# Kernel tuning notes

Hardware: AMD Instinct MI355X
Metric: run time of the kernel (lower is better)

The kernel has to match this reference:

```python
import jax, jax.numpy as jnp
import numpy as np

EPS = 1e-5  # BatchNorm2d default eps


def setup_inputs() -> dict:
    key = jax.random.key(0)
    k1, k2, k3, k4 = jax.random.split(key, 4)
    B, C, S, E = 2, 512, 256, 512  # C == E is required by the module's math
    x = jax.random.normal(k1, (B, C, S, E), dtype=jnp.float32)
    Q = jax.random.normal(k2, (E, E), dtype=jnp.float32)
    K = jax.random.normal(k3, (E, E), dtype=jnp.float32)
    V = jax.random.normal(k4, (E, E), dtype=jnp.float32)
    return {"x": x, "Q": Q, "K": K, "V": V}


def reference(x, Q, K, V):
    # BatchNorm2d(affine=False), training-mode batch stats over (B, H, W)
    mean = jnp.mean(x, axis=(0, 2, 3), keepdims=True)
    var = jnp.var(x, axis=(0, 2, 3), keepdims=True)  # biased, matches torch normalization
    xn = (x - mean) * jax.lax.rsqrt(var + EPS)

    divisor = jnp.sqrt(jnp.asarray(x.shape[-1], dtype=x.dtype))
    q = jnp.einsum('bcse,ef->bcsf', xn, Q)
    k = jnp.einsum('bcse,ef->bcsf', xn, K)
    v = jnp.einsum('bcse,ef->bcsf', xn, V)

    # scores: [B, C, S, S]
    prod = jnp.einsum('bcsf,bctf->bcst', q, k) / divisor
    # nn.Softmax2d softmaxes over the CHANNEL dim (axis 1)
    sm = jax.nn.softmax(prod, axis=1)
    attention = jnp.einsum('bcst,bctf->bcsf', sm, v)
    # dropout is identity in eval/reference mode; residual since E_in == E_out
    return attention + xn
```

## Files before the change

kernel.cpp:

```cpp
#include <hip/hip_runtime.h>
#include <hip/hip_bf16.h>
#include <cstdio>

#define Bn 2
#define Cn 512
#define Sn 256
#define En 512

typedef __attribute__((ext_vector_type(8))) short bf16x8;
typedef __attribute__((ext_vector_type(4))) float f32x4;

static constexpr size_t PROD_B = (1ull << 20);
static constexpr size_t V_B    = PROD_B + (256ull << 20);
static constexpr size_t ATH_B  = V_B + (256ull << 20);
static constexpr size_t ATL_B  = ATH_B + (512ull << 10);
static constexpr size_t VT_B   = ATL_B + (512ull << 10);
static constexpr size_t XNH_B  = VT_B + (512ull << 10);
static constexpr size_t XNL_B  = XNH_B + (256ull << 20);
static constexpr size_t WS_BIG = XNL_B + (256ull << 20);
static constexpr size_t SMT_B  = XNL_B;

__device__ __forceinline__ unsigned short f2bf(float f) {
  union { __hip_bfloat16 h; unsigned short u; } cv;
  cv.h = __float2bfloat16(f);
  return cv.u;
}
__device__ __forceinline__ float bf2f(unsigned short u) {
  union { unsigned int i; float f; } cv;
  cv.i = ((unsigned int)u) << 16;
  return cv.f;
}
__device__ __forceinline__ void split2(float v, unsigned short& h, unsigned short& l) {
  h = f2bf(v);
  l = f2bf(v - bf2f(h));
}
__device__ __forceinline__ bf16x8 ldfrag(const unsigned short* arr, int row, int ks, int lane) {
  const int byte = (ks * 64 + ((lane >> 4) << 4)) ^ ((row & 7) << 4);
  return *(const bf16x8*)((const char*)(arr + (size_t)row * 64) + byte);
}
__device__ __forceinline__ f32x4 MFMA(bf16x8 a, bf16x8 b, f32x4 c) {
  return __builtin_amdgcn_mfma_f32_16x16x32_bf16(a, b, c, 0, 0, 0);
}
__device__ __forceinline__ void glds16(const void* g, void* l) {
  __builtin_amdgcn_global_load_lds(
      (const __attribute__((address_space(1))) unsigned int*)g,
      (__attribute__((address_space(3))) unsigned int*)l, 16, 0, 0);
}
__device__ __forceinline__ void stage_tile(const unsigned short* g, unsigned short* l,
                                           int nbytes, int wid, int lane, int nwaves) {
  const char* gb = (const char*)g;
  char* lb = (char*)l;
  for (int j = wid; j < (nbytes >> 10); j += nwaves)
    glds16(gb + j * 1024 + lane * 16, lb + j * 1024);
}

__global__ void k1_stats(const float* __restrict__ x, float* __restrict__ ws) {
  const int c = blockIdx.x, tid = threadIdx.x;
  const float4* p0 = (const float4*)(x + (size_t)c * (Sn * En));
  const float4* p1 = (const float4*)(x + (size_t)(Cn + c) * (Sn * En));
  float s1 = 0.f, s2 = 0.f;
  for (int i = tid; i < (Sn * En / 4); i += 256) {
    float4 a = p0[i], b = p1[i];
    s1 += (a.x + a.y) + (a.z + a.w) + (b.x + b.y) + (b.z + b.w);
    s2 += (a.x * a.x + a.y * a.y) + (a.z * a.z + a.w * a.w) +
          (b.x * b.x + b.y * b.y) + (b.z * b.z + b.w * b.w);
  }
  __shared__ float r1[256], r2[256];
  r1[tid] = s1; r2[tid] = s2;
  __syncthreads();
  for (int off = 128; off > 0; off >>= 1) {
    if (tid < off) { r1[tid] += r1[tid + off]; r2[tid] += r2[tid + off]; }
    __syncthreads();
  }
  if (tid == 0) {
    const float n = (float)(2 * Sn * En);
    float mean = r1[0] / n;
    float var = r2[0] / n - mean * mean;
    ws[c] = mean;
    ws[512 + c] = 1.0f / sqrtf(var + 1e-5f);
  }
}

__global__ void kA(const float* __restrict__ Q, const float* __restrict__ K,
                   const float* __restrict__ V, unsigned short* __restrict__ ATh,
                   unsigned short* __restrict__ ATl, unsigned short* __restrict__ VT) {
  const int f = blockIdx.x, tid = threadIdx.x;
  __shared__ float Kf[512];
  for (int i = tid; i < 512; i += 256) Kf[i] = K[(size_t)f * 512 + i];
  __syncthreads();
  const int fr64 = f & 63;
  const size_t atbase = ((size_t)(f >> 6) * 8) * 4096 + (size_t)fr64 * 64;
  const size_t vtbase = ((size_t)(f >> 7) * 8) * 8192 + (size_t)(f & 127) * 64;
#pragma unroll
  for (int half = 0; half < 2; ++half) {
    const int e = tid + half * 256;
    const float* Qe = Q + (size_t)e * 512;
    float acc = 0.f;
    for (int t = 0; t < 512; t += 4) {
      float4 q = *(const float4*)(Qe + t);
      acc += q.x * Kf[t] + q.y * Kf[t + 1] + q.z * Kf[t + 2] + q.w * Kf[t + 3];
    }
    unsigned short h, l;
    split2(acc, h, l);
    const int et = e >> 6, ec = e & 63;
    const int swa = (ec & 3) | ((ec & 60) ^ ((fr64 & 7) << 3));
    ATh[atbase + (size_t)et * 4096 + swa] = h;
    ATl[atbase + (size_t)et * 4096 + swa] = l;
    const int swv = (ec & 3) | ((ec & 60) ^ ((f & 7) << 3));
    VT[vtbase + (size_t)et * 8192 + swv] = f2bf(V[(size_t)e * 512 + f]);
  }
}

__global__ void kxn(const float* __restrict__ x, const float* __restrict__ ws,
                    unsigned short* __restrict__ XNh, unsigned short* __restrict__ XNl) {
  const int bid = blockIdx.x;
  const int bc = bid >> 1, half = bid & 1;
  const int c = bc & 511;
  const float mean = ws[c], rstd = ws[512 + c];
  const float* xb = x + (size_t)bc * 131072 + (size_t)half * 128 * 512;
  const int tid = threadIdx.x;
#pragma unroll 4
  for (int i = 0; i < 64; ++i) {
    const int g = tid + i * 256;
    const int r = g >> 7, c4 = g & 127;
    const float4 xv = *(const float4*)(xb + (size_t)r * 512 + c4 * 4);
    ushort4 hv, lv;
    split2((xv.x - mean) * rstd, hv.x, lv.x);
    split2((xv.y - mean) * rstd, hv.y, lv.y);
    split2((xv.z - mean) * rstd, hv.z, lv.z);
    split2((xv.w - mean) * rstd, hv.w, lv.w);
    const int et = c4 >> 4, colt4 = c4 & 15;
    const int row = half * 128 + r;
    const size_t idx = ((size_t)(bc * 8 + et) * 256 + row) * 64 +
                       ((colt4 * 4) ^ ((row & 7) << 3));
    *(ushort4*)&XNh[idx] = hv;
    *(ushort4*)&XNl[idx] = lv;
  }
}

__launch_bounds__(256)
__global__ void kv_proj(const unsigned short* __restrict__ VT,
                        const unsigned short* __restrict__ XNh_g,
                        unsigned short* __restrict__ vT_out) {
  __shared__ unsigned short BUF[2][16384];
  const int bid = blockIdx.x;
  const int L = (bid & 7) * 1024 + (bid >> 3);
  const int bc = L >> 3;
  const int fq = (L >> 1) & 3;
  const int th = L & 1;
  const int f0 = fq * 128, t0 = th * 128;
  const int tid = threadIdx.x, w = tid >> 6, lane = tid & 63;

  f32x4 acc[2][8];
#pragma unroll
  for (int i = 0; i < 2; ++i)
#pragma unroll
    for (int j = 0; j < 8; ++j) acc[i][j] = (f32x4){0.f, 0.f, 0.f, 0.f};

  stage_tile(VT + ((size_t)fq * 8 + 0) * 8192, &BUF[0][0], 16384, w, lane, 4);
  stage_tile(XNh_g + ((size_t)(bc * 8 + 0) * 256 + t0) * 64, &BUF[0][8192], 16384, w, lane, 4);
  __syncthreads();
#pragma unroll 1
  for (int et = 0; et < 8; ++et) {
    if (et < 7) {
      const int b = (et + 1) & 1;
      stage_tile(VT + ((size_t)fq * 8 + et + 1) * 8192, &BUF[b][0], 16384, w, lane, 4);
      stage_tile(XNh_g + ((size_t)(bc * 8 + et + 1) * 256 + t0) * 64, &BUF[b][8192],
                 16384, w, lane, 4);
    }
    const unsigned short* cb = &BUF[et & 1][0];
#pragma unroll
    for (int ks = 0; ks < 2; ++ks) {
      bf16x8 a0 = ldfrag(cb, w * 32 + (lane & 15), ks, lane);
      bf16x8 a1 = ldfrag(cb, w * 32 + 16 + (lane & 15), ks, lane);
#pragma unroll
      for (int ct = 0; ct < 8; ++ct) {
        bf16x8 b = ldfrag(cb + 8192, ct * 16 + (lane & 15), ks, lane);
        acc[0][ct] = MFMA(a0, b, acc[0][ct]);
        acc[1][ct] = MFMA(a1, b, acc[1][ct]);
      }
    }
    __syncthreads();
  }
#pragma unroll
  for (int rt = 0; rt < 2; ++rt)
#pragma unroll
    for (int ct = 0; ct < 8; ++ct)
#pragma unroll
      for (int r = 0; r < 4; ++r) {
        const int f = f0 + w * 32 + rt * 16 + (lane >> 4) * 4 + r;
        const int t = t0 + ct * 16 + (lane & 15);
        const size_t idx = (((size_t)bc * 4 + (f >> 7)) * 4 + (t >> 6)) * 8192 +
                           (size_t)(f & 127) * 64 +
                           ((t & 3) | ((t & 60) ^ ((f & 7) << 3)));
        vT_out[idx] = f2bf(acc[rt][ct][r]);
      }
}

__launch_bounds__(512)
__global__ void kscores(const unsigned short* __restrict__ ATh_g,
                        const unsigned short* __restrict__ ATl_g,
                        const unsigned short* __restrict__ XNh_g,
                        const unsigned short* __restrict__ XNl_g,
                        float* __restrict__ prod) {
  __shared__ unsigned short ATS[32768];
  __shared__ unsigned short XNS[32768];
  __shared__ unsigned short YS[8][1024];
  const int bid = blockIdx.x;
  const int L = (bid & 7) * 256 + (bid >> 3);
  const int bc = L >> 1, half = L & 1;
  float* prodc = prod + (size_t)bc * 65536 + (size_t)half * 128 * 256;
  const int tid = threadIdx.x, w = tid >> 6, lane = tid & 63;
  const int lr = lane & 15, lk = lane >> 4;

  const int arow = half * 128 + w * 16 + lr;
  const unsigned short* xnh_row = XNh_g + ((size_t)bc * 8 * 256 + arow) * 64;
  const unsigned short* xnl_row = XNl_g + ((size_t)bc * 8 * 256 + arow) * 64;
  const int ac0 = ((lk * 8)) ^ ((arow & 7) << 3);
  const int ac1 = (32 + lk * 8) ^ ((arow & 7) << 3);

  f32x4 accz[16];
#pragma unroll
  for (int i = 0; i < 16; ++i) accz[i] = (f32x4){0.f, 0.f, 0.f, 0.f};
  f32x4 accy[2];
  unsigned short* const ys = &YS[w][0];

  auto stATS = [&](int j) {
    const int ft64 = j >> 1, hf = (j & 1) * 2048;
    const char* gh = (const char*)(ATh_g + ((size_t)ft64 * 8 + w) * 4096 + hf);
    const char* gl = (const char*)(ATl_g + ((size_t)ft64 * 8 + w) * 4096 + hf);
    char* dh = (char*)(ATS + w * 2048);
    char* dl = (char*)(ATS + 16384 + w * 2048);
#pragma unroll
    for (int r = 0; r < 4; ++r) {
      glds16(gh + r * 1024 + lane * 16, dh + r * 1024);
      glds16(gl + r * 1024 + lane * 16, dl + r * 1024);
    }
  };
  auto stXNS = [&](int fe) {
    const char* gh = (const char*)(XNh_g + (size_t)(bc * 8 + fe) * 16384);
    const char* gl = (const char*)(XNl_g + (size_t)(bc * 8 + fe) * 16384);
#pragma unroll
    for (int r = 0; r < 4; ++r) {
      glds16(gh + (w * 4 + r) * 1024 + lane * 16, (char*)XNS + (w * 4 + r) * 1024);
      glds16(gl + (w * 4 + r) * 1024 + lane * 16, (char*)(XNS + 16384) + (w * 4 + r) * 1024);
    }
  };
  auto ph1 = [&]() {
#pragma unroll 2
    for (int et = 0; et < 8; ++et) {
      const unsigned short* ATSh = ATS + et * 2048;
      const unsigned short* ATSl = ATS + 16384 + et * 2048;
#pragma unroll
      for (int ks = 0; ks < 2; ++ks) {
        const int ac = (ks ? ac1 : ac0);
        const bf16x8 ah = *(const bf16x8*)(xnh_row + (size_t)et * 16384 + ac);
        const bf16x8 al = *(const bf16x8*)(xnl_row + (size_t)et * 16384 + ac);
#pragma unroll
        for (int fc = 0; fc < 2; ++fc) {
          bf16x8 bh = ldfrag(ATSh, fc * 16 + lr, ks, lane);
          bf16x8 bl = ldfrag(ATSl, fc * 16 + lr, ks, lane);
          accy[fc] = MFMA(ah, bh, accy[fc]);
          accy[fc] = MFMA(ah, bl, accy[fc]);
          accy[fc] = MFMA(al, bh, accy[fc]);
        }
      }
    }
  };
  auto ywrite = [&]() {
#pragma unroll
    for (int fc = 0; fc < 2; ++fc)
#pragma unroll
      for (int r = 0; r < 4; ++r) {
        unsigned short h, l;
        split2(accy[fc][r], h, l);
        const int idx = (lk * 4 + r) * 32 + fc * 16 + lr;
        ys[idx] = h;
        ys[512 + idx] = l;
      }
  };
  auto ph2 = [&](int j) {
    const int jo = (j & 1) * 64;
    const bf16x8 yh = *(const bf16x8*)((const char*)ys + lr * 64 + lk * 16);
    const bf16x8 yl = *(const bf16x8*)((const char*)ys + 1024 + lr * 64 + lk * 16);
#pragma unroll
    for (int ct = 0; ct < 16; ++ct) {
      const int t = ct * 16 + lr;
      const int byte = (jo + lk * 16) ^ ((t & 7) << 4);
      const bf16x8 bh = *(const bf16x8*)((const char*)(XNS + (size_t)t * 64) + byte);
      const bf16x8 bl = *(const bf16x8*)((const char*)(XNS + 16384 + (size_t)t * 64) + byte);
      accz[ct] = MFMA(yh, bh, accz[ct]);
      accz[ct] = MFMA(yh, bl, accz[ct]);
      accz[ct] = MFMA(yl, bh, accz[ct]);
    }
  };

  stXNS(0);
  stATS(0);
  __syncthreads();

#pragma unroll 1
  for (int fe = 0; fe < 8; ++fe) {
    accy[0] = (f32x4){0.f, 0.f, 0.f, 0.f};
    accy[1] = (f32x4){0.f, 0.f, 0.f, 0.f};
    ph1();
    ywrite();
    __syncthreads();
    stATS(2 * fe + 1);
    ph2(2 * fe);
    __syncthreads();
    accy[0] = (f32x4){0.f, 0.f, 0.f, 0.f};
    accy[1] = (f32x4){0.f, 0.f, 0.f, 0.f};
    ph1();
    ywrite();
    __syncthreads();
    if (fe < 7) stATS(2 * fe + 2);
    ph2(2 * fe + 1);
    __syncthreads();
    if (fe < 7) stXNS(fe + 1);
  }

  const float scale = 0.044194173824159216f;
#pragma unroll
  for (int ct = 0; ct < 16; ++ct)
#pragma unroll
    for (int r = 0; r < 4; ++r) {
      const int row = w * 16 + lk * 4 + r;
      prodc[(size_t)row * 256 + ct * 16 + lr] = accz[ct][r] * scale;
    }
}

__launch_bounds__(512)
__global__ void k3_softmax(const float* __restrict__ prodf, unsigned short* __restrict__ smT) {
  const int bid = blockIdx.x;
  const int b = bid >> 8, s = bid & 255;
  const int tid = threadIdx.x;
  const int t = tid & 255, ch = tid >> 8;
  const float* __restrict__ p =
      prodf + (size_t)b * (512ull * 65536) + (size_t)s * 256 + t + (size_t)ch * 256 * 65536;
  float m = -3.4e38f, sum = 0.f;
#pragma unroll 4
  for (int cc = 0; cc < 256; ++cc) {
    const float v = p[(size_t)cc * 65536];
    if (v > m) { sum *= __expf(m - v); m = v; }
    sum += __expf(v - m);
  }
  __shared__ float Ms[2][256], Ss[2][256];
  Ms[ch][t] = m; Ss[ch][t] = sum;
  __syncthreads();
  const float mo = Ms[ch ^ 1][t], so = Ss[ch ^ 1][t];
  const float mm = fmaxf(m, mo);
  const float inv = 1.0f / (sum * __expf(m - mm) + so * __expf(mo - mm));
  const int sh = s >> 7, r = s & 127, kt = t >> 6, col = t & 63;
  const int cidx = r * 64 + ((col & 3) | ((col & 60) ^ ((r & 7) << 3)));
  const size_t tbase = ((size_t)b * 512 + ch * 256) * 2 + sh;
#pragma unroll 4
  for (int cc = 0; cc < 256; ++cc) {
    const float ev = __expf(p[(size_t)cc * 65536] - mm) * inv;
    smT[((tbase + (size_t)cc * 2) * 4 + kt) * 8192 + cidx] = f2bf(ev);
  }
}

__launch_bounds__(256)
__global__ void k4_pv(const unsigned short* __restrict__ XNh_g,
                      const unsigned short* __restrict__ vT,
                      const unsigned short* __restrict__ smT,
                      float* __restrict__ out) {
  __shared__ unsigned short BUF[2][16384];
  const int bid = blockIdx.x;
  const int L = (bid & 7) * 1024 + (bid >> 3);
  const int bc = L >> 3;
  const int sh = (L >> 2) & 1;
  const int fh = L & 3;
  const int s0 = sh * 128, f0 = fh * 128;
  const int tid = threadIdx.x, w = tid >> 6, lane = tid & 63;

  f32x4 acc[2][8];
#pragma unroll
  for (int i = 0; i < 2; ++i)
#pragma unroll
    for (int j = 0; j < 8; ++j) acc[i][j] = (f32x4){0.f, 0.f, 0.f, 0.f};

  stage_tile(smT + (((size_t)bc * 2 + sh) * 4 + 0) * 8192, &BUF[0][0], 16384, w, lane, 4);
  stage_tile(vT + (((size_t)bc * 4 + fh) * 4 + 0) * 8192, &BUF[0][8192], 16384, w, lane, 4);
  __syncthreads();
#pragma unroll 1
  for (int kt = 0; kt < 4; ++kt) {
    if (kt < 3) {
      const int b = (kt + 1) & 1;
      stage_tile(smT + (((size_t)bc * 2 + sh) * 4 + kt + 1) * 8192, &BUF[b][0],
                 16384, w, lane, 4);
      stage_tile(vT + (((size_t)bc * 4 + fh) * 4 + kt + 1) * 8192, &BUF[b][8192],
                 16384, w, lane, 4);
    }
    const unsigned short* cb = &BUF[kt & 1][0];
#pragma unroll
    for (int ks = 0; ks < 2; ++ks) {
      bf16x8 a0 = ldfrag(cb, w * 32 + (lane & 15), ks, lane);
      bf16x8 a1 = ldfrag(cb, w * 32 + 16 + (lane & 15), ks, lane);
#pragma unroll
      for (int ct = 0; ct < 8; ++ct) {
        bf16x8 b = ldfrag(cb + 8192, ct * 16 + (lane & 15), ks, lane);
        acc[0][ct] = MFMA(a0, b, acc[0][ct]);
        acc[1][ct] = MFMA(a1, b, acc[1][ct]);
      }
    }
    __syncthreads();
  }
  const int lr = lane & 15, lk = lane >> 4;
#pragma unroll
  for (int rt = 0; rt < 2; ++rt)
#pragma unroll
    for (int ct = 0; ct < 8; ++ct)
#pragma unroll
      for (int r = 0; r < 4; ++r) {
        const int srow = s0 + w * 32 + rt * 16 + lk * 4 + r;
        const int fcol = f0 + ct * 16 + lr;
        const int et = fcol >> 6, col = fcol & 63;
        const unsigned short xh = XNh_g[((size_t)(bc * 8 + et) * 256 + srow) * 64 +
                                        ((col & 3) | ((col & 60) ^ ((srow & 7) << 3)))];
        const size_t oi = (size_t)bc * 131072 + (size_t)srow * 512 + fcol;
        out[oi] = acc[rt][ct][r] + bf2f(xh);
      }
}

extern "C" void kernel_launch(void* const* d_in, const int* in_sizes, int n_in,
                              void* d_out, int out_size, void* d_ws, size_t ws_size,
                              hipStream_t stream) {
  const float* x = (const float*)d_in[0];
  const float* Q = (const float*)d_in[1];
  const float* K = (const float*)d_in[2];
  const float* V = (const float*)d_in[3];
  float* out = (float*)d_out;
  float* ws = (float*)d_ws;
  float* prodf = (float*)((char*)d_ws + PROD_B);
  unsigned short* vT   = (unsigned short*)((char*)d_ws + V_B);
  unsigned short* ATh  = (unsigned short*)((char*)d_ws + ATH_B);
  unsigned short* ATl  = (unsigned short*)((char*)d_ws + ATL_B);
  unsigned short* VTm  = (unsigned short*)((char*)d_ws + VT_B);
  unsigned short* XNh  = (unsigned short*)((char*)d_ws + XNH_B);
  unsigned short* XNl  = (unsigned short*)((char*)d_ws + XNL_B);
  unsigned short* smT  = (unsigned short*)((char*)d_ws + SMT_B);
  if (ws_size < WS_BIG) {
    fprintf(stderr, "kernel_launch: ws_size %zu < needed %zu — expect corruption\n",
            ws_size, WS_BIG);
  }
  k1_stats<<<dim3(512), dim3(256), 0, stream>>>(x, ws);
  kA<<<dim3(512), dim3(256), 0, stream>>>(Q, K, V, ATh, ATl, VTm);
  kxn<<<dim3(2048), dim3(256), 0, stream>>>(x, ws, XNh, XNl);
  kv_proj<<<dim3(8192), dim3(256), 0, stream>>>(VTm, XNh, vT);
  kscores<<<dim3(2048), dim3(512), 0, stream>>>(ATh, ATl, XNh, XNl, prodf);
  k3_softmax<<<dim3(512), dim3(512), 0, stream>>>(prodf, smT);
  k4_pv<<<dim3(8192), dim3(256), 0, stream>>>(XNh, vT, smT, out);
}
```

Measured before the change: 2.317 ms.

## Restructure kscores: double-buffer XN tiles, read AT from global, widen per-wave f-chunk

The scores kernel no longer stages the A^T weight tiles in shared memory. Each wave reads its B fragments directly from global/L2 and computes a 64-wide f chunk per pass instead of 32. The XN tile is now double-buffered in LDS, so the next tile is prefetched during compute, and the per-wave Y scratch uses a swizzled layout with priority raised around the MFMA loop. This removes about three of the four barriers per iteration and overlaps staging with math, at the cost of more global-load traffic and latency for the weight fragments plus doubled XN LDS usage.

```diff
diff --git a/kernel.cpp b/kernel.cpp
--- a/kernel.cpp
+++ b/kernel.cpp
@@ -203,8 +203,7 @@
                         const unsigned short* __restrict__ XNh_g,
                         const unsigned short* __restrict__ XNl_g,
                         float* __restrict__ prod) {
-  __shared__ unsigned short ATS[32768];
-  __shared__ unsigned short XNS[32768];
+  __shared__ unsigned short XNS[2][32768];
   __shared__ unsigned short YS[8][1024];
   const int bid = blockIdx.x;
   const int L = (bid & 7) * 256 + (bid >> 3);
@@ -216,108 +215,82 @@
   const int arow = half * 128 + w * 16 + lr;
   const unsigned short* xnh_row = XNh_g + ((size_t)bc * 8 * 256 + arow) * 64;
   const unsigned short* xnl_row = XNl_g + ((size_t)bc * 8 * 256 + arow) * 64;
-  const int ac0 = ((lk * 8)) ^ ((arow & 7) << 3);
+  const int ac0 = (lk * 8) ^ ((arow & 7) << 3);
   const int ac1 = (32 + lk * 8) ^ ((arow & 7) << 3);
+  const int brswz = (lr & 7) << 3;
 
   f32x4 accz[16];
 #pragma unroll
   for (int i = 0; i < 16; ++i) accz[i] = (f32x4){0.f, 0.f, 0.f, 0.f};
-  f32x4 accy[2];
+  f32x4 accy[4];
   unsigned short* const ys = &YS[w][0];
 
-  auto stATS = [&](int j) {
-    const int ft64 = j >> 1, hf = (j & 1) * 2048;
-    const char* gh = (const char*)(ATh_g + ((size_t)ft64 * 8 + w) * 4096 + hf);
-    const char* gl = (const char*)(ATl_g + ((size_t)ft64 * 8 + w) * 4096 + hf);
-    char* dh = (char*)(ATS + w * 2048);
-    char* dl = (char*)(ATS + 16384 + w * 2048);
-#pragma unroll
-    for (int r = 0; r < 4; ++r) {
-      glds16(gh + r * 1024 + lane * 16, dh + r * 1024);
-      glds16(gl + r * 1024 + lane * 16, dl + r * 1024);
-    }
+  auto stXNS = [&](int ft, int p) {
+    stage_tile(XNh_g + (size_t)(bc * 8 + ft) * 16384, &XNS[p][0], 32768, w, lane, 8);
+    stage_tile(XNl_g + (size_t)(bc * 8 + ft) * 16384, &XNS[p][16384], 32768, w, lane, 8);
   };
-  auto stXNS = [&](int fe) {
-    const char* gh = (const char*)(XNh_g + (size_t)(bc * 8 + fe) * 16384);
-    const char* gl = (const char*)(XNl_g + (size_t)(bc * 8 + fe) * 16384);
-#pragma unroll
-    for (int r = 0; r < 4; ++r) {
-      glds16(gh + (w * 4 + r) * 1024 + lane * 16, (char*)XNS + (w * 4 + r) * 1024);
-      glds16(gl + (w * 4 + r) * 1024 + lane * 16, (char*)(XNS + 16384) + (w * 4 + r) * 1024);
-    }
-  };
-  auto ph1 = [&]() {
+
+  stXNS(0, 0);
+  __syncthreads();
+
+#pragma unroll 1
+  for (int ft = 0; ft < 8; ++ft) {
+    if (ft < 7) stXNS(ft + 1, (ft + 1) & 1);
+#pragma unroll
+    for (int i = 0; i < 4; ++i) accy[i] = (f32x4){0.f, 0.f, 0.f, 0.f};
+
 #pragma unroll 2
     for (int et = 0; et < 8; ++et) {
-      const unsigned short* ATSh = ATS + et * 2048;
-      const unsigned short* ATSl = ATS + 16384 + et * 2048;
+      const unsigned short* ATh_t = ATh_g + ((size_t)ft * 8 + et) * 4096;
+      const unsigned short* ATl_t = ATl_g + ((size_t)ft * 8 + et) * 4096;
 #pragma unroll
       for (int ks = 0; ks < 2; ++ks) {
-        const int ac = (ks ? ac1 : ac0);
+        const int ac = ks ? ac1 : ac0;
         const bf16x8 ah = *(const bf16x8*)(xnh_row + (size_t)et * 16384 + ac);
         const bf16x8 al = *(const bf16x8*)(xnl_row + (size_t)et * 16384 + ac);
-#pragma unroll
-        for (int fc = 0; fc < 2; ++fc) {
-          bf16x8 bh = ldfrag(ATSh, fc * 16 + lr, ks, lane);
-          bf16x8 bl = ldfrag(ATSl, fc * 16 + lr, ks, lane);
+        const int bko = (ks * 32 + lk * 8) ^ brswz;
+#pragma unroll
+        for (int fc = 0; fc < 4; ++fc) {
+          const int bidx = (fc * 16 + lr) * 64 + bko;
+          const bf16x8 bh = *(const bf16x8*)(ATh_t + bidx);
+          const bf16x8 bl = *(const bf16x8*)(ATl_t + bidx);
           accy[fc] = MFMA(ah, bh, accy[fc]);
           accy[fc] = MFMA(ah, bl, accy[fc]);
           accy[fc] = MFMA(al, bh, accy[fc]);
         }
       }
     }
-  };
-  auto ywrite = [&]() {
-#pragma unroll
-    for (int fc = 0; fc < 2; ++fc)
-#pragma unroll
-      for (int r = 0; r < 4; ++r) {
-        unsigned short h, l;
-        split2(accy[fc][r], h, l);
-        const int idx = (lk * 4 + r) * 32 + fc * 16 + lr;
-        ys[idx] = h;
-        ys[512 + idx] = l;
-      }
-  };
-  auto ph2 = [&](int j) {
-    const int jo = (j & 1) * 64;
-    const bf16x8 yh = *(const bf16x8*)((const char*)ys + lr * 64 + lk * 16);
-    const bf16x8 yl = *(const bf16x8*)((const char*)ys + 1024 + lr * 64 + lk * 16);
-#pragma unroll
-    for (int ct = 0; ct < 16; ++ct) {
-      const int t = ct * 16 + lr;
-      const int byte = (jo + lk * 16) ^ ((t & 7) << 4);
-      const bf16x8 bh = *(const bf16x8*)((const char*)(XNS + (size_t)t * 64) + byte);
-      const bf16x8 bl = *(const bf16x8*)((const char*)(XNS + 16384 + (size_t)t * 64) + byte);
-      accz[ct] = MFMA(yh, bh, accz[ct]);
-      accz[ct] = MFMA(yh, bl, accz[ct]);
-      accz[ct] = MFMA(yl, bh, accz[ct]);
-    }
-  };
-
-  stXNS(0);
-  stATS(0);
-  __syncthreads();
-
-#pragma unroll 1
-  for (int fe = 0; fe < 8; ++fe) {
-    accy[0] = (f32x4){0.f, 0.f, 0.f, 0.f};
-    accy[1] = (f32x4){0.f, 0.f, 0.f, 0.f};
-    ph1();
-    ywrite();
+
+    const unsigned short* XH = &XNS[ft & 1][0];
+    const unsigned short* XL = &XNS[ft & 1][16384];
+#pragma unroll
+    for (int fh2 = 0; fh2 < 2; ++fh2) {
+#pragma unroll
+      for (int fc2 = 0; fc2 < 2; ++fc2)
+#pragma unroll
+        for (int r = 0; r < 4; ++r) {
+          unsigned short h, l;
+          split2(accy[fh2 * 2 + fc2][r], h, l);
+          const int row = lk * 4 + r, col = fc2 * 16 + lr;
+          const int idx = row * 32 + ((col & 7) | ((col & 24) ^ ((row & 3) << 3)));
+          ys[idx] = h;
+          ys[512 + idx] = l;
+        }
+      const int yoff = lr * 32 + ((lk * 8) ^ ((lr & 3) << 3));
+      const bf16x8 yh = *(const bf16x8*)(ys + yoff);
+      const bf16x8 yl = *(const bf16x8*)(ys + 512 + yoff);
+      __builtin_amdgcn_s_setprio(1);
+#pragma unroll
+      for (int ct = 0; ct < 16; ++ct) {
+        const bf16x8 bh = ldfrag(XH, ct * 16 + lr, fh2, lane);
+        const bf16x8 bl = ldfrag(XL, ct * 16 + lr, fh2, lane);
+        accz[ct] = MFMA(yh, bh, accz[ct]);
+        accz[ct] = MFMA(yh, bl, accz[ct]);
+        accz[ct] = MFMA(yl, bh, accz[ct]);
+      }
+      __builtin_amdgcn_s_setprio(0);
+    }
     __syncthreads();
-    stATS(2 * fe + 1);
-    ph2(2 * fe);
-    __syncthreads();
-    accy[0] = (f32x4){0.f, 0.f, 0.f, 0.f};
-    accy[1] = (f32x4){0.f, 0.f, 0.f, 0.f};
-    ph1();
-    ywrite();
-    __syncthreads();
-    if (fe < 7) stATS(2 * fe + 2);
-    ph2(2 * fe + 1);
-    __syncthreads();
-    if (fe < 7) stXNS(fe + 1);
   }
 
   const float scale = 0.044194173824159216f;
```

Result: no change. 2.325 ms (+0.3%).
